# Kernel optimization log

Hardware: AMD Instinct MI355X
Metric: run time of the kernel (lower is better)

Reference implementation:

```python
import jax, jax.numpy as jnp
import numpy as np

G = 128  # voxel grid extent per axis (positions are integer voxel coords in [0, G))
K = 3    # kernel size per axis -> 27 offsets


def setup_inputs() -> dict:
    key = jax.random.key(0)
    k1, k2, k3 = jax.random.split(key, 3)
    N, Cin, Cout = 500000, 32, 32
    features = jax.random.normal(k1, (N, Cin), dtype=jnp.float32)
    in_positions = jax.random.randint(k2, (N, 3), 0, G, dtype=jnp.int32)
    # learned conv weight: one [Cin, Cout] matrix per kernel offset (27 total)
    weight = jax.random.normal(k3, (K ** 3, Cin, Cout), dtype=jnp.float32) * 0.05
    return {"features": features, "in_positions": in_positions, "weight": weight}


def _hash(pos):
    # unique linear key for integer voxel coords in [0, G)^3
    return (pos[:, 0] * G + pos[:, 1]) * G + pos[:, 2]


def reference(features, in_positions, weight):
    # Submanifold sparse conv (kernel 3x3x3, odd -> offset 0, out_positions == in_positions,
    # voxel_size = 1.0, no bias, no normalize):
    # for each active voxel, gather active neighbors at each of the 27 kernel offsets,
    # transform with the per-offset weight matrix, and accumulate.
    N = features.shape[0]
    # dense hash table: voxel key -> row index in features, -1 if inactive
    table = jnp.full((G * G * G,), -1, dtype=jnp.int32)
    table = table.at[_hash(in_positions)].set(jnp.arange(N, dtype=jnp.int32))

    out = jnp.zeros((N, weight.shape[-1]), dtype=features.dtype)
    r = K // 2
    k = 0
    for dx in range(-r, r + 1):
        for dy in range(-r, r + 1):
            for dz in range(-r, r + 1):
                npos = in_positions + jnp.array([dx, dy, dz], dtype=jnp.int32)
                inside = jnp.all((npos >= 0) & (npos < G), axis=1)
                idx = table[jnp.where(inside, _hash(npos), 0)]
                valid = inside & (idx >= 0)
                # gather active neighbor features; zero where neighbor inactive
                gathered = jnp.where(valid[:, None], features[jnp.maximum(idx, 0)], 0.0)
                out = out + gathered @ weight[k]  # [N, Cout]
                k += 1
    return out
```

## Files before the change

### kernel.cpp

```cpp
#include <hip/hip_runtime.h>


#define GRID 128
#define CIN 32
#define COUT 32
#define NOFF 27

typedef __attribute__((ext_vector_type(8))) short bf16x8;
typedef __attribute__((ext_vector_type(4))) float f32x4;

__device__ inline unsigned short f2bf(float x) {
    union { float f; unsigned u; } v; v.f = x;
    unsigned r = v.u + 0x7fff + ((v.u >> 16) & 1);
    return (unsigned short)(r >> 16);
}

__global__ void prep_kernel(const float* __restrict__ feats,
                            const int* __restrict__ pos,
                            const float* __restrict__ wt,
                            int* __restrict__ table,
                            unsigned* __restrict__ featsB,
                            unsigned short* __restrict__ wtT,
                            int N, int elems4) {
    int i = blockIdx.x * 256 + threadIdx.x;
    if (i < elems4) {
        float4 v = *(const float4*)(feats + 4 * (size_t)i);
        unsigned lo = (unsigned)f2bf(v.x) | ((unsigned)f2bf(v.y) << 16);
        unsigned hi = (unsigned)f2bf(v.z) | ((unsigned)f2bf(v.w) << 16);
        uint2 o; o.x = lo; o.y = hi;
        *(uint2*)(featsB + 2 * (size_t)i) = o;
    }
    if (i < N) {
        int x = pos[3 * i], y = pos[3 * i + 1], z = pos[3 * i + 2];
        atomicMax(&table[(x * GRID + y) * GRID + z], i);
    }
    if (i < NOFF * CIN * COUT) {
        int k = i >> 10, r = i & 1023, ci = r >> 5, co = r & 31;
        wtT[k * 1024 + co * 32 + ci] = f2bf(wt[i]);
    }
}

__global__ __launch_bounds__(1024, 8)
void conv_kernel(const unsigned short* __restrict__ featsB,
                 const int* __restrict__ pos,
                 const unsigned short* __restrict__ wtT,
                 const int* __restrict__ table,
                 float* __restrict__ out, int N) {
    __shared__ __align__(16) unsigned short ldsw[NOFF * 1024];

    int tid = threadIdx.x;
    int wave = tid >> 6, lane = tid & 63;
    int m = lane & 15, quad = lane >> 4;
    int tile = blockIdx.x * 16 + wave;
    int base = tile * 16;
    int g = base + m;
    bool gv = g < N;

    int x = 0, y = 0, z = 0;
    if (gv) { x = pos[3 * g]; y = pos[3 * g + 1]; z = pos[3 * g + 2]; }
    int h = (x * GRID + y) * GRID + z;
    bool v0[3] = {gv && x > 0, gv, gv && x < GRID - 1};
    bool v1[3] = {gv && y > 0, gv, gv && y < GRID - 1};
    bool v2[3] = {gv && z > 0, gv, gv && z < GRID - 1};

    int ids[NOFF];
#pragma unroll
    for (int k = 0; k < NOFF; ++k) {
        const int dx = k / 9, dy = (k / 3) % 3, dz = k % 3;
        bool ok = v0[dx] && v1[dy] && v2[dz];
        int hk = h + (dx - 1) * GRID * GRID + (dy - 1) * GRID + (dz - 1);
        hk = ok ? hk : 0;
        int id = table[hk];
        ids[k] = ok ? id : -1;
    }

    {
        const uint4* src = (const uint4*)wtT;
        uint4* dst = (uint4*)ldsw;
        for (int e = tid; e < NOFF * 1024 * 2 / 16; e += 1024)
            dst[e] = src[e];
    }
    __syncthreads();

    f32x4 acc0 = {0.f, 0.f, 0.f, 0.f};
    f32x4 acc1 = {0.f, 0.f, 0.f, 0.f};
    const unsigned short* wb = ldsw + m * 32 + quad * 8;

#pragma unroll
    for (int k = 0; k < NOFF; ++k) {
        int id = ids[k];
        int row = (id >= 0 ? id : 0) * CIN;
        bf16x8 a = *(const bf16x8*)(featsB + row + quad * 8);
        if (id < 0) a = (bf16x8){0, 0, 0, 0, 0, 0, 0, 0};

        bf16x8 b0 = *(const bf16x8*)(wb + k * 1024);
        bf16x8 b1 = *(const bf16x8*)(wb + k * 1024 + 512);

        acc0 = __builtin_amdgcn_mfma_f32_16x16x32_bf16(a, b0, acc0, 0, 0, 0);
        acc1 = __builtin_amdgcn_mfma_f32_16x16x32_bf16(a, b1, acc1, 0, 0, 0);
    }

#pragma unroll
    for (int i = 0; i < 4; ++i) {
        int p = base + quad * 4 + i;
        if (p < N) {
            out[(size_t)p * COUT + m]      = acc0[i];
            out[(size_t)p * COUT + m + 16] = acc1[i];
        }
    }
}

extern "C" void kernel_launch(void* const* d_in, const int* in_sizes, int n_in,
                              void* d_out, int out_size, void* d_ws, size_t ws_size,
                              hipStream_t stream) {
    const float* feats = (const float*)d_in[0];
    const int*   pos   = (const int*)d_in[1];
    const float* wt    = (const float*)d_in[2];
    float* out = (float*)d_out;
    int N = in_sizes[0] / CIN;

    char* ws = (char*)d_ws;
    int* table = (int*)ws;
    size_t table_bytes = (size_t)GRID * GRID * GRID * sizeof(int);
    unsigned short* wtT = (unsigned short*)(ws + table_bytes);
    unsigned short* featsB = (unsigned short*)(ws + table_bytes + 65536);

    hipMemsetAsync(table, 0xFF, table_bytes, stream);

    int elems4 = N * CIN / 4;
    prep_kernel<<<(elems4 + 255) / 256, 256, 0, stream>>>(
        feats, pos, wt, table, (unsigned*)featsB, wtT, N, elems4);

    int numTiles = (N + 15) / 16;
    int blocks = (numTiles + 15) / 16;
    conv_kernel<<<blocks, 1024, 0, stream>>>(featsB, pos, wtT, table, out, N);
}
```

Before: 256.0 us.

## Convert features to bf16 inside conv kernel and reorder weight layout in LDS

Drops the separate full-feature fp32-to-bf16 pre-pass. The conv kernel now gathers fp32 neighbor rows directly and converts them in registers, which avoids writing and rereading a bf16 copy of all features. The cost is that each gather reads twice as many bytes per neighbor, and there are 27 gathers per voxel. The weight transpose is also changed to a blocked layout so each lane's LDS reads are contiguous, aiming to reduce bank conflicts.

```diff
diff --git a/kernel.cpp b/kernel.cpp
--- a/kernel.cpp
+++ b/kernel.cpp
@@ -1,4 +1,5 @@
 #include <hip/hip_runtime.h>
+#include <hip/hip_bf16.h>
 
 
 #define GRID 128
@@ -15,33 +16,24 @@
     return (unsigned short)(r >> 16);
 }
 
-__global__ void prep_kernel(const float* __restrict__ feats,
-                            const int* __restrict__ pos,
+__global__ void prep_kernel(const int* __restrict__ pos,
                             const float* __restrict__ wt,
                             int* __restrict__ table,
-                            unsigned* __restrict__ featsB,
-                            unsigned short* __restrict__ wtT,
-                            int N, int elems4) {
+                            unsigned short* __restrict__ wtT, int N) {
     int i = blockIdx.x * 256 + threadIdx.x;
-    if (i < elems4) {
-        float4 v = *(const float4*)(feats + 4 * (size_t)i);
-        unsigned lo = (unsigned)f2bf(v.x) | ((unsigned)f2bf(v.y) << 16);
-        unsigned hi = (unsigned)f2bf(v.z) | ((unsigned)f2bf(v.w) << 16);
-        uint2 o; o.x = lo; o.y = hi;
-        *(uint2*)(featsB + 2 * (size_t)i) = o;
-    }
     if (i < N) {
         int x = pos[3 * i], y = pos[3 * i + 1], z = pos[3 * i + 2];
         atomicMax(&table[(x * GRID + y) * GRID + z], i);
     }
     if (i < NOFF * CIN * COUT) {
         int k = i >> 10, r = i & 1023, ci = r >> 5, co = r & 31;
-        wtT[k * 1024 + co * 32 + ci] = f2bf(wt[i]);
+        int idx = k * 1024 + (co >> 4) * 512 + (ci >> 3) * 128 + (co & 15) * 8 + (ci & 7);
+        wtT[idx] = f2bf(wt[i]);
     }
 }
 
 __global__ __launch_bounds__(1024, 8)
-void conv_kernel(const unsigned short* __restrict__ featsB,
+void conv_kernel(const float* __restrict__ feats,
                  const int* __restrict__ pos,
                  const unsigned short* __restrict__ wtT,
                  const int* __restrict__ table,
@@ -84,20 +76,28 @@
 
     f32x4 acc0 = {0.f, 0.f, 0.f, 0.f};
     f32x4 acc1 = {0.f, 0.f, 0.f, 0.f};
-    const unsigned short* wb = ldsw + m * 32 + quad * 8;
+    const unsigned short* wb = ldsw + (quad * 16 + m) * 8;
 
 #pragma unroll
     for (int k = 0; k < NOFF; ++k) {
         int id = ids[k];
         int row = (id >= 0 ? id : 0) * CIN;
-        bf16x8 a = *(const bf16x8*)(featsB + row + quad * 8);
-        if (id < 0) a = (bf16x8){0, 0, 0, 0, 0, 0, 0, 0};
+        const float* f = feats + (size_t)row + quad * 8;
+        float4 f0 = *(const float4*)f;
+        float4 f1 = *(const float4*)(f + 4);
+
+        union { bf16x8 v; __hip_bfloat162 h2[4]; } a;
+        a.h2[0] = __float22bfloat162_rn(make_float2(f0.x, f0.y));
+        a.h2[1] = __float22bfloat162_rn(make_float2(f0.z, f0.w));
+        a.h2[2] = __float22bfloat162_rn(make_float2(f1.x, f1.y));
+        a.h2[3] = __float22bfloat162_rn(make_float2(f1.z, f1.w));
+        if (id < 0) a.v = (bf16x8){0, 0, 0, 0, 0, 0, 0, 0};
 
         bf16x8 b0 = *(const bf16x8*)(wb + k * 1024);
         bf16x8 b1 = *(const bf16x8*)(wb + k * 1024 + 512);
 
-        acc0 = __builtin_amdgcn_mfma_f32_16x16x32_bf16(a, b0, acc0, 0, 0, 0);
-        acc1 = __builtin_amdgcn_mfma_f32_16x16x32_bf16(a, b1, acc1, 0, 0, 0);
+        acc0 = __builtin_amdgcn_mfma_f32_16x16x32_bf16(a.v, b0, acc0, 0, 0, 0);
+        acc1 = __builtin_amdgcn_mfma_f32_16x16x32_bf16(a.v, b1, acc1, 0, 0, 0);
     }
 
 #pragma unroll
@@ -123,15 +123,13 @@
     int* table = (int*)ws;
     size_t table_bytes = (size_t)GRID * GRID * GRID * sizeof(int);
     unsigned short* wtT = (unsigned short*)(ws + table_bytes);
-    unsigned short* featsB = (unsigned short*)(ws + table_bytes + 65536);
 
     hipMemsetAsync(table, 0xFF, table_bytes, stream);
 
-    int elems4 = N * CIN / 4;
-    prep_kernel<<<(elems4 + 255) / 256, 256, 0, stream>>>(
-        feats, pos, wt, table, (unsigned*)featsB, wtT, N, elems4);
+    int pthreads = (N > NOFF * CIN * COUT) ? N : NOFF * CIN * COUT;
+    prep_kernel<<<(pthreads + 255) / 256, 256, 0, stream>>>(pos, wt, table, wtT, N);
 
     int numTiles = (N + 15) / 16;
     int blocks = (numTiles + 15) / 16;
-    conv_kernel<<<blocks, 1024, 0, stream>>>(featsB, pos, wtT, table, out, N);
+    conv_kernel<<<blocks, 1024, 0, stream>>>(feats, pos, wtT, table, out, N);
 }
```

Measured after the change: 280.0 us. 1.09x slower.
